# Kernel tuning notes

Hardware: AMD Instinct MI355X
Metric: run time of the kernel (lower is better)

## Reference

```python
import jax, jax.numpy as jnp
import numpy as np

N, E, F, H, G, C = 50000, 800000, 768, 256, 512, 2  # H = nhid*2 (nhid=128), G graphs, C classes
NHID = 128


def setup_inputs() -> dict:
    key = jax.random.key(0)
    ks = jax.random.split(key, 18)
    s = 0.05
    x = jax.random.normal(ks[0], (N, F), jnp.float32)
    edge_index = jax.random.randint(ks[1], (2, E), 0, N, dtype=jnp.int32)
    # sorted batch vector; every graph non-empty so the 'first node per graph' gather is valid
    batch = ((jnp.arange(N) * G) // N).astype(jnp.int32)
    return {
        "x": x,
        "edge_index": edge_index,
        "batch": batch,
        # GATConv 1 (in=F, out=H, heads=1)
        "W1": jax.random.normal(ks[2], (F, H), jnp.float32) * s,
        "as1": jax.random.normal(ks[3], (H,), jnp.float32) * s,
        "ad1": jax.random.normal(ks[4], (H,), jnp.float32) * s,
        "b1": jnp.zeros((H,), jnp.float32),
        # GATConv 2 (in=H, out=H)
        "W2": jax.random.normal(ks[5], (H, H), jnp.float32) * s,
        "as2": jax.random.normal(ks[6], (H,), jnp.float32) * s,
        "ad2": jax.random.normal(ks[7], (H,), jnp.float32) * s,
        "b2": jnp.zeros((H,), jnp.float32),
        # fc0: num_features -> nhid (news branch)
        "W0": jax.random.normal(ks[8], (F, NHID), jnp.float32) * s,
        "b0": jnp.zeros((NHID,), jnp.float32),
        # fc1: 2*nhid -> nhid (used twice, as in the source)
        "Wf1": jax.random.normal(ks[9], (H, NHID), jnp.float32) * s,
        "bf1": jnp.zeros((NHID,), jnp.float32),
        # fc2: nhid -> num_classes
        "Wf2": jax.random.normal(ks[10], (NHID, C), jnp.float32) * s,
        "bf2": jnp.zeros((C,), jnp.float32),
    }


def _gat(x, src, dst, W, a_s, a_d, b):
    # PyG GATConv, heads=1, concat=True, negative_slope=0.2, self-loops pre-appended to src/dst.
    h = x @ W                                   # [N, H]
    e = jax.nn.leaky_relu((h @ a_s)[src] + (h @ a_d)[dst], 0.2)  # [E+N]
    m = jax.ops.segment_max(e, dst, num_segments=N)
    ex = jnp.exp(e - m[dst])                    # stable segment softmax numerator
    denom = jax.ops.segment_sum(ex, dst, num_segments=N)
    agg = jax.ops.segment_sum(ex[:, None] * h[src], dst, num_segments=N)  # [N, H]
    return agg / denom[:, None] + b


def reference(x, edge_index, batch, W1, as1, ad1, b1, W2, as2, ad2, b2, W0, b0, Wf1, bf1, Wf2, bf2):
    loop = jnp.arange(N, dtype=edge_index.dtype)
    src = jnp.concatenate([edge_index[0], loop])  # add self-loops (PyG default)
    dst = jnp.concatenate([edge_index[1], loop])
    h = jax.nn.selu(_gat(x, src, dst, W1, as1, ad1, b1))
    h = jax.nn.selu(_gat(h, src, dst, W2, as2, ad2, b2))
    # global mean pool over graphs
    cnt = jax.ops.segment_sum(jnp.ones((N,), h.dtype), batch, num_segments=G)
    pooled = jax.nn.selu(jax.ops.segment_sum(h, batch, num_segments=G) / cnt[:, None])
    z = jax.nn.selu(pooled @ Wf1 + bf1)
    # dropout(p=0.5) in eval mode -> identity
    # concat branch: first node of each graph (news root)
    first_idx = jax.ops.segment_min(jnp.arange(N), batch, num_segments=G)
    news = jax.nn.relu(x[first_idx] @ W0 + b0)
    z = jnp.concatenate([z, news], axis=1)       # [G, 2*nhid]
    z = jax.nn.relu(z @ Wf1 + bf1)
    return jax.nn.log_softmax(z @ Wf2 + bf2, axis=-1)
```

## Files before the change

kernel.cpp:

```cpp
#include <hip/hip_runtime.h>
#include <hip/hip_bf16.h>
#include <cstdint>
#include <cstddef>

#define NN 50000
#define EE 800000
#define FF 768
#define HH 256
#define GG 512
#define CC 2
#define NHIDD 128
#define ETOT (EE + NN)
#define NCHUNK 49

typedef __attribute__((ext_vector_type(8))) short bf16x8;
typedef __attribute__((ext_vector_type(4))) float f32x4;
typedef __attribute__((ext_vector_type(8))) unsigned short us8;

__device__ __forceinline__ float b2f(unsigned short u){
  union { float f; uint32_t i; } v; v.i = ((uint32_t)u) << 16; return v.f;
}
__device__ __forceinline__ unsigned short f2b(float f){
  uint32_t u = __float_as_uint(f);
  uint32_t r = (u + 0x7fffu + ((u >> 16) & 1u)) >> 16;
  return (unsigned short)r;
}
__device__ __forceinline__ uint32_t cvtpk(float a, float b){
  uint32_t d;
  asm volatile("v_cvt_pk_bf16_f32 %0, %1, %2" : "=v"(d) : "v"(a), "v"(b));
  return d;
}
__device__ __forceinline__ float selu_f(float x){
  const float lam = 1.0507009873554805f, alp = 1.6732632423543772f;
  return x > 0.f ? lam * x : lam * alp * (__expf(x) - 1.f);
}

__device__ __forceinline__ void gload_lds16(const void* g, void* l){
  __builtin_amdgcn_global_load_lds((const __attribute__((address_space(1))) void*)g,
                                   (__attribute__((address_space(3))) void*)l, 16, 0, 0);
}

__global__ __launch_bounds__(256) void swizzleW2(const float* __restrict__ W1, const float* __restrict__ W2,
                                                 unsigned short* __restrict__ Wsw1, unsigned short* __restrict__ Wsw2){
  int i = blockIdx.x * 256 + threadIdx.x;
  if (i < FF * HH){
    int k = i / HH, n = i % HH;
    Wsw1[(size_t)(k >> 5) * 8192 + n * 32 + (k & 31)] = f2b(W1[i]);
  } else {
    int i2 = i - FF * HH;
    int k = i2 / HH, n = i2 % HH;
    Wsw2[(size_t)(k >> 5) * 8192 + n * 32 + (k & 31)] = f2b(W2[i2]);
  }
}

__global__ __launch_bounds__(256) void deg_kernel(const int* __restrict__ dstA, int* __restrict__ deg){
  int i = blockIdx.x * 256 + threadIdx.x;
  if (i < ETOT){
    int d = (i < EE) ? dstA[i] : (i - EE);
    atomicAdd(&deg[d], 1);
  }
}

__global__ __launch_bounds__(256) void scanA(const int* __restrict__ deg, int* __restrict__ bsum){
  __shared__ int red[256];
  int c = blockIdx.x, tid = threadIdx.x;
  int base = c * 1024 + tid * 4;
  int s = 0;
#pragma unroll
  for (int j = 0; j < 4; j++){ int idx = base + j; if (idx < NN) s += deg[idx]; }
  red[tid] = s; __syncthreads();
  for (int off = 128; off > 0; off >>= 1){
    if (tid < off) red[tid] += red[tid + off];
    __syncthreads();
  }
  if (tid == 0) bsum[c] = red[0];
}

__global__ __launch_bounds__(256) void scanC(const int* __restrict__ deg, const int* __restrict__ bsum,
                                             int* __restrict__ row_ptr, int* __restrict__ fill_ptr){
  __shared__ int ts[256];
  __shared__ int cbase;
  int c = blockIdx.x, tid = threadIdx.x;
  int pb = (tid < c) ? bsum[tid] : 0;
  ts[tid] = pb; __syncthreads();
  for (int off = 128; off > 0; off >>= 1){
    if (tid < off) ts[tid] += ts[tid + off];
    __syncthreads();
  }
  if (tid == 0) cbase = ts[0];
  __syncthreads();
  int base = c * 1024 + tid * 4;
  int v[4]; int s = 0;
#pragma unroll
  for (int j = 0; j < 4; j++){ int idx = base + j; v[j] = (idx < NN) ? deg[idx] : 0; s += v[j]; }
  ts[tid] = s; __syncthreads();
  for (int off = 1; off < 256; off <<= 1){
    int add = (tid >= off) ? ts[tid - off] : 0;
    __syncthreads();
    ts[tid] += add;
    __syncthreads();
  }
  int run = ts[tid] - s + cbase;
#pragma unroll
  for (int j = 0; j < 4; j++){
    int idx = base + j;
    if (idx < NN){ row_ptr[idx] = run; fill_ptr[idx] = run; }
    run += v[j];
  }
  if (c == 0 && tid == 0) row_ptr[NN] = ETOT;
}

__global__ __launch_bounds__(256) void fill_kernel(const int* __restrict__ srcA, const int* __restrict__ dstA,
                                                   int* __restrict__ fill_ptr, int* __restrict__ csr_src){
  int i = blockIdx.x * 256 + threadIdx.x;
  if (i < ETOT){
    int s = (i < EE) ? srcA[i] : (i - EE);
    int d = (i < EE) ? dstA[i] : (i - EE);
    int pos = atomicAdd(&fill_ptr[d], 1);
    csr_src[pos] = s;
  }
}

__global__ __launch_bounds__(512, 4) void gemm1_f32(const float* __restrict__ A,
                                                 const unsigned short* __restrict__ Wsw,
                                                 const float* __restrict__ a_s, const float* __restrict__ a_d,
                                                 unsigned short* __restrict__ out,
                                                 float* __restrict__ als, float* __restrict__ ald, int M){
  __shared__ float Alf[32 * 384];
  const int tid = threadIdx.x;
  const int m0 = blockIdx.x * 32;
  const int lane = tid & 63, w = tid >> 6;
  const int koff = (lane >> 4) * 8;
  const int arow = lane & 15;
  const int nrow = w * 32 + (lane & 15);

  f32x4 acc[2][2];
#pragma unroll
  for (int rt = 0; rt < 2; rt++)
#pragma unroll
    for (int ct = 0; ct < 2; ct++) acc[rt][ct] = (f32x4){0.f, 0.f, 0.f, 0.f};

  const unsigned short* bbase = Wsw + ((size_t)nrow * 32 + koff);
  bf16x8 bcur[2][2];

  auto stage_half = [&](int p){
#pragma unroll
    for (int j = 0; j < 6; j++){
      int L16 = j * 512 + tid;
      int row = L16 / 96;
      int ch  = L16 - row * 96;
      int sch = ch ^ (row & 7);
      int gr  = m0 + row; if (gr >= M) gr = M - 1;
      gload_lds16(A + (size_t)gr * FF + p * 384 + sch * 4,
                  Alf + (size_t)(j * 512 + w * 64) * 4);
    }
  };

#pragma unroll
  for (int p = 0; p < 2; p++){
    if (p == 1) __syncthreads();
    stage_half(p);
#pragma unroll
    for (int k2 = 0; k2 < 2; k2++)
#pragma unroll
      for (int ct = 0; ct < 2; ct++)
        bcur[k2][ct] = *(const bf16x8*)(bbase + (size_t)(p * 12 + k2) * 8192 + ct * 512);
    __syncthreads();

    for (int ks = 0; ks < 6; ks++){
      bf16x8 bnext[2][2];
      if (ks + 1 < 6){
#pragma unroll
        for (int k2 = 0; k2 < 2; k2++)
#pragma unroll
          for (int ct = 0; ct < 2; ct++)
            bnext[k2][ct] = *(const bf16x8*)(bbase + (size_t)(p * 12 + (ks + 1) * 2 + k2) * 8192 + ct * 512);
      }
      bf16x8 af[2][2];
#pragma unroll
      for (int k2 = 0; k2 < 2; k2++)
#pragma unroll
        for (int rt = 0; rt < 2; rt++){
          int R = rt * 16 + arow;
          int c = ks * 16 + k2 * 8 + (lane >> 4) * 2;
          int m = R & 7;
          float4 v0 = *(const float4*)&Alf[R * 384 + ((c)     ^ m) * 4];
          float4 v1 = *(const float4*)&Alf[R * 384 + ((c + 1) ^ m) * 4];
          union { bf16x8 v; uint32_t u[4]; } X;
          X.u[0] = cvtpk(v0.x, v0.y); X.u[1] = cvtpk(v0.z, v0.w);
          X.u[2] = cvtpk(v1.x, v1.y); X.u[3] = cvtpk(v1.z, v1.w);
          af[k2][rt] = X.v;
        }
#pragma unroll
      for (int k2 = 0; k2 < 2; k2++)
#pragma unroll
        for (int rt = 0; rt < 2; rt++)
#pragma unroll
          for (int ct = 0; ct < 2; ct++)
            acc[rt][ct] = __builtin_amdgcn_mfma_f32_16x16x32_bf16(af[k2][rt], bcur[k2][ct], acc[rt][ct], 0, 0, 0);
      if (ks + 1 < 6){
#pragma unroll
        for (int k2 = 0; k2 < 2; k2++)
#pragma unroll
          for (int ct = 0; ct < 2; ct++) bcur[k2][ct] = bnext[k2][ct];
      }
    }
  }

#pragma unroll
  for (int rt = 0; rt < 2; rt++){
    int mbase = m0 + rt * 16 + (lane >> 4) * 4;
#pragma unroll
    for (int r = 0; r < 4; r++){
      int m = mbase + r;
      if (m < M){
        size_t ro = (size_t)m * HH + w * 32 + (lane & 15);
        out[ro + 0]  = f2b(acc[rt][0][r]);
        out[ro + 16] = f2b(acc[rt][1][r]);
      }
    }
  }

  float as_c[2], ad_c[2];
#pragma unroll
  for (int ct = 0; ct < 2; ct++){
    int col = w * 32 + ct * 16 + (lane & 15);
    as_c[ct] = a_s[col]; ad_c[ct] = a_d[col];
  }
  float ps[2][4], pd[2][4];
#pragma unroll
  for (int rt = 0; rt < 2; rt++)
#pragma unroll
    for (int r = 0; r < 4; r++){
      float s = 0.f, d = 0.f;
#pragma unroll
      for (int ct = 0; ct < 2; ct++){ float v = acc[rt][ct][r]; s += v * as_c[ct]; d += v * ad_c[ct]; }
      ps[rt][r] = s; pd[rt][r] = d;
    }
#pragma unroll
  for (int off = 1; off < 16; off <<= 1){
#pragma unroll
    for (int rt = 0; rt < 2; rt++)
#pragma unroll
      for (int r = 0; r < 4; r++){
        ps[rt][r] += __shfl_xor(ps[rt][r], off);
        pd[rt][r] += __shfl_xor(pd[rt][r], off);
      }
  }
  __syncthreads();
  float* red = Alf;
  if ((lane & 15) == 0){
    int q = lane >> 4;
#pragma unroll
    for (int rt = 0; rt < 2; rt++)
#pragma unroll
      for (int r = 0; r < 4; r++){
        int row = rt * 16 + q * 4 + r;
        red[w * 32 + row]       = ps[rt][r];
        red[256 + w * 32 + row] = pd[rt][r];
      }
  }
  __syncthreads();
  if (tid < 32){
    float s = 0.f, d = 0.f;
#pragma unroll
    for (int ww = 0; ww < 8; ww++){
      s += red[ww * 32 + tid];
      d += red[256 + ww * 32 + tid];
    }
    int m = m0 + tid;
    if (m < M){ als[m] = s; ald[m] = d; }
  }
}

template<int K, int MINW>
__global__ __launch_bounds__(256, MINW) void gemm_mfma(const unsigned short* __restrict__ A,
                                                 const unsigned short* __restrict__ Wsw,
                                                 const float* __restrict__ a_s, const float* __restrict__ a_d,
                                                 unsigned short* __restrict__ out,
                                                 float* __restrict__ als, float* __restrict__ ald, int M){
  constexpr int CHROW = K / 8;
  __shared__ unsigned short Al[32 * K];
  const int tid = threadIdx.x;
  const int m0 = blockIdx.x * 32;
  const int lane = tid & 63, w = tid >> 6;
  const int koff = (lane >> 4) * 8;
  const int arow = lane & 15;
  const int nrow = w * 64 + (lane & 15);

  f32x4 acc[2][4];
#pragma unroll
  for (int rt = 0; rt < 2; rt++)
#pragma unroll
    for (int ct = 0; ct < 4; ct++) acc[rt][ct] = (f32x4){0.f, 0.f, 0.f, 0.f};

  constexpr int ROUNDS = (32 * CHROW) / 256;
#pragma unroll
  for (int j = 0; j < ROUNDS; j++){
    int L16 = j * 256 + tid;
    int row = L16 / CHROW;
    int ch  = L16 - row * CHROW;
    int sch = ch ^ (row & 7);
    int gr  = m0 + row; if (gr >= M) gr = M - 1;
    gload_lds16(A + (size_t)gr * K + sch * 8,
                &Al[(size_t)(j * 256 + w * 64) * 8]);
  }

  const unsigned short* bbase = Wsw + ((size_t)nrow * 32 + koff);
  bf16x8 bcur[2][4];
#pragma unroll
  for (int k2 = 0; k2 < 2; k2++)
#pragma unroll
    for (int ct = 0; ct < 4; ct++)
      bcur[k2][ct] = *(const bf16x8*)(bbase + (size_t)k2 * 8192 + ct * 512);

  __syncthreads();

  constexpr int NIT = K / 64;
  for (int ks = 0; ks < NIT; ks++){
    bf16x8 bnext[2][4];
    if (ks + 1 < NIT){
#pragma unroll
      for (int k2 = 0; k2 < 2; k2++)
#pragma unroll
        for (int ct = 0; ct < 4; ct++)
          bnext[k2][ct] = *(const bf16x8*)(bbase + (size_t)((ks + 1) * 2 + k2) * 8192 + ct * 512);
    }
    bf16x8 af[2][2];
#pragma unroll
    for (int k2 = 0; k2 < 2; k2++)
#pragma unroll
      for (int rt = 0; rt < 2; rt++){
        int R = rt * 16 + arow;
        int chb = (ks * 8 + k2 * 4 + (lane >> 4)) ^ (R & 7);
        af[k2][rt] = *(const bf16x8*)&Al[(size_t)R * K + chb * 8];
      }
#pragma unroll
    for (int k2 = 0; k2 < 2; k2++)
#pragma unroll
      for (int rt = 0; rt < 2; rt++)
#pragma unroll
        for (int ct = 0; ct < 4; ct++)
          acc[rt][ct] = __builtin_amdgcn_mfma_f32_16x16x32_bf16(af[k2][rt], bcur[k2][ct], acc[rt][ct], 0, 0, 0);
    if (ks + 1 < NIT){
#pragma unroll
      for (int k2 = 0; k2 < 2; k2++)
#pragma unroll
        for (int ct = 0; ct < 4; ct++) bcur[k2][ct] = bnext[k2][ct];
    }
  }

#pragma unroll
  for (int rt = 0; rt < 2; rt++){
    int mbase = m0 + rt * 16 + (lane >> 4) * 4;
#pragma unroll
    for (int r = 0; r < 4; r++){
      int m = mbase + r;
      if (m < M){
        size_t ro = (size_t)m * HH + w * 64 + (lane & 15);
        out[ro + 0]  = f2b(acc[rt][0][r]);
        out[ro + 16] = f2b(acc[rt][1][r]);
        out[ro + 32] = f2b(acc[rt][2][r]);
        out[ro + 48] = f2b(acc[rt][3][r]);
      }
    }
  }

  float as_c[4], ad_c[4];
#pragma unroll
  for (int ct = 0; ct < 4; ct++){
    int col = w * 64 + ct * 16 + (lane & 15);
    as_c[ct] = a_s[col]; ad_c[ct] = a_d[col];
  }
  float ps[2][4], pd[2][4];
#pragma unroll
  for (int rt = 0; rt < 2; rt++)
#pragma unroll
    for (int r = 0; r < 4; r++){
      float s = 0.f, d = 0.f;
#pragma unroll
      for (int ct = 0; ct < 4; ct++){ float v = acc[rt][ct][r]; s += v * as_c[ct]; d += v * ad_c[ct]; }
      ps[rt][r] = s; pd[rt][r] = d;
    }
#pragma unroll
  for (int off = 1; off < 16; off <<= 1){
#pragma unroll
    for (int rt = 0; rt < 2; rt++)
#pragma unroll
      for (int r = 0; r < 4; r++){
        ps[rt][r] += __shfl_xor(ps[rt][r], off);
        pd[rt][r] += __shfl_xor(pd[rt][r], off);
      }
  }
  __syncthreads();
  float* red = (float*)Al;
  if ((lane & 15) == 0){
    int q = lane >> 4;
#pragma unroll
    for (int rt = 0; rt < 2; rt++)
#pragma unroll
      for (int r = 0; r < 4; r++){
        int row = rt * 16 + q * 4 + r;
        red[w * 32 + row]       = ps[rt][r];
        red[128 + w * 32 + row] = pd[rt][r];
      }
  }
  __syncthreads();
  if (tid < 32){
    float s = red[tid] + red[32 + tid] + red[64 + tid] + red[96 + tid];
    float d = red[128 + tid] + red[160 + tid] + red[192 + tid] + red[224 + tid];
    int m = m0 + tid;
    if (m < M){ als[m] = s; ald[m] = d; }
  }
}

__global__ __launch_bounds__(256) void agg_wave(const unsigned short* __restrict__ h,
    const float* __restrict__ als, const float* __restrict__ ald,
    const int* __restrict__ row_ptr, const int* __restrict__ csr_src,
    const float* __restrict__ bias, unsigned short* __restrict__ outp){
  int node = blockIdx.x * 4 + (threadIdx.x >> 6);
  int lane = threadIdx.x & 63;
  if (node >= NN) return;
  int base = row_ptr[node];
  int deg  = row_ptr[node + 1] - base;
  float aldd = ald[node];
  float den = 0.f;
  float a[8] = {0.f, 0.f, 0.f, 0.f, 0.f, 0.f, 0.f, 0.f};
  const int f8 = (lane & 31) * 8;
  const int half = lane >> 5;
  for (int p0 = 0; p0 < deg; p0 += 64){
    int cnt = min(64, deg - p0);
    float ev = 0.f; int s = 0;
    if (lane < cnt){
      s = csr_src[base + p0 + lane];
      float v = als[s] + aldd;
      v = v > 0.f ? v : 0.2f * v;
      ev = __expf(v);
    }
    den += ev;
    int j = 0;
    for (; j + 8 <= cnt; j += 8){
      int j0 = j + half, j1 = j + 2 + half, j2 = j + 4 + half, j3 = j + 6 + half;
      int s0 = __shfl(s, j0), s1 = __shfl(s, j1), s2 = __shfl(s, j2), s3 = __shfl(s, j3);
      float e0 = __shfl(ev, j0), e1 = __shfl(ev, j1), e2 = __shfl(ev, j2), e3 = __shfl(ev, j3);
      us8 g0 = *(const us8*)&h[(size_t)s0 * HH + f8];
      us8 g1 = *(const us8*)&h[(size_t)s1 * HH + f8];
      us8 g2 = *(const us8*)&h[(size_t)s2 * HH + f8];
      us8 g3 = *(const us8*)&h[(size_t)s3 * HH + f8];
#pragma unroll
      for (int i = 0; i < 8; i++) a[i] += e0 * b2f(g0[i]) + e1 * b2f(g1[i]);
#pragma unroll
      for (int i = 0; i < 8; i++) a[i] += e2 * b2f(g2[i]) + e3 * b2f(g3[i]);
    }
    for (; j + 4 <= cnt; j += 4){
      int j0 = j + half, j1 = j + 2 + half;
      int s0 = __shfl(s, j0), s1 = __shfl(s, j1);
      float e0 = __shfl(ev, j0), e1 = __shfl(ev, j1);
      us8 g0 = *(const us8*)&h[(size_t)s0 * HH + f8];
      us8 g1 = *(const us8*)&h[(size_t)s1 * HH + f8];
#pragma unroll
      for (int i = 0; i < 8; i++) a[i] += e0 * b2f(g0[i]) + e1 * b2f(g1[i]);
    }
    for (; j < cnt; j += 2){
      int jj = j + half;
      int sj = __shfl(s, jj & 63);
      float ejr = __shfl(ev, jj & 63);
      float ej = (jj < cnt) ? ejr : 0.f;
      us8 gj = *(const us8*)&h[(size_t)sj * HH + f8];
#pragma unroll
      for (int i = 0; i < 8; i++) a[i] += ej * b2f(gj[i]);
    }
  }
  for (int off = 32; off > 0; off >>= 1) den += __shfl_xor(den, off);
#pragma unroll
  for (int i = 0; i < 8; i++) a[i] += __shfl_xor(a[i], 32);
  if (lane < 32){
    float inv = 1.f / den;
    float4 b4a = *(const float4*)&bias[f8];
    float4 b4b = *(const float4*)&bias[f8 + 4];
    us8 o;
    o[0] = f2b(selu_f(a[0] * inv + b4a.x));
    o[1] = f2b(selu_f(a[1] * inv + b4a.y));
    o[2] = f2b(selu_f(a[2] * inv + b4a.z));
    o[3] = f2b(selu_f(a[3] * inv + b4a.w));
    o[4] = f2b(selu_f(a[4] * inv + b4b.x));
    o[5] = f2b(selu_f(a[5] * inv + b4b.y));
    o[6] = f2b(selu_f(a[6] * inv + b4b.z));
    o[7] = f2b(selu_f(a[7] * inv + b4b.w));
    *(us8*)&outp[(size_t)node * HH + f8] = o;
  }
}

__global__ __launch_bounds__(256) void head_kernel(const unsigned short* __restrict__ x3,
    const int* __restrict__ batch, const float* __restrict__ x,
    const float* __restrict__ W0, const float* __restrict__ b0,
    const float* __restrict__ Wf1, const float* __restrict__ bf1,
    const float* __restrict__ Wf2, const float* __restrict__ bf2,
    float* __restrict__ out){
  __shared__ float pr[HH];
  __shared__ float xr[FF];
  __shared__ float zc[HH];
  __shared__ int se[2];
  __shared__ float l0s[2], l1s[2];
  int g = blockIdx.x, t = threadIdx.x;
  if (t < 2){
    int target = g + t, lo = 0, hi = NN;
    while (lo < hi){ int mid = (lo + hi) >> 1; if (batch[mid] < target) lo = mid + 1; else hi = mid; }
    se[t] = lo;
  }
  __syncthreads();
  int s = se[0], e = se[1];
  {
    float acc = 0.f;
    for (int n = s; n < e; n++) acc += b2f(x3[(size_t)n * HH + t]);
    pr[t] = selu_f(acc / (float)(e - s));
  }
  for (int k = t; k < FF; k += 256) xr[k] = x[(size_t)s * FF + k];
  __syncthreads();
  if (t < NHIDD){
    float acc = 0.f;
    for (int k = 0; k < HH; k++) acc += pr[k] * Wf1[k * NHIDD + t];
    zc[t] = selu_f(acc + bf1[t]);
  } else {
    int t2 = t - NHIDD;
    float acc = 0.f;
    for (int k = 0; k < FF; k++) acc += xr[k] * W0[k * NHIDD + t2];
    acc += b0[t2];
    zc[NHIDD + t2] = acc > 0.f ? acc : 0.f;
  }
  __syncthreads();
  if (t < NHIDD){
    float acc = 0.f;
    for (int k = 0; k < HH; k++) acc += zc[k] * Wf1[k * NHIDD + t];
    float z2 = acc + bf1[t]; z2 = z2 > 0.f ? z2 : 0.f;
    float p0 = z2 * Wf2[t * CC + 0];
    float p1 = z2 * Wf2[t * CC + 1];
    for (int off = 32; off > 0; off >>= 1){ p0 += __shfl_xor(p0, off); p1 += __shfl_xor(p1, off); }
    if ((t & 63) == 0){ l0s[t >> 6] = p0; l1s[t >> 6] = p1; }
  }
  __syncthreads();
  if (t == 0){
    float l0 = l0s[0] + l0s[1] + bf2[0];
    float l1 = l1s[0] + l1s[1] + bf2[1];
    float mx = fmaxf(l0, l1);
    float lse = mx + logf(__expf(l0 - mx) + __expf(l1 - mx));
    out[g * CC + 0] = l0 - lse;
    out[g * CC + 1] = l1 - lse;
  }
}

extern "C" void kernel_launch(void* const* d_in, const int* in_sizes, int n_in,
                              void* d_out, int out_size, void* d_ws, size_t ws_size,
                              hipStream_t stream){
  const float* x          = (const float*)d_in[0];
  const int* edge_index   = (const int*)d_in[1];
  const int* batch        = (const int*)d_in[2];
  const float* W1  = (const float*)d_in[3];
  const float* as1 = (const float*)d_in[4];
  const float* ad1 = (const float*)d_in[5];
  const float* b1  = (const float*)d_in[6];
  const float* W2  = (const float*)d_in[7];
  const float* as2 = (const float*)d_in[8];
  const float* ad2 = (const float*)d_in[9];
  const float* b2  = (const float*)d_in[10];
  const float* W0  = (const float*)d_in[11];
  const float* b0  = (const float*)d_in[12];
  const float* Wf1 = (const float*)d_in[13];
  const float* bf1 = (const float*)d_in[14];
  const float* Wf2 = (const float*)d_in[15];
  const float* bf2 = (const float*)d_in[16];
  float* out = (float*)d_out;

  char* w = (char*)d_ws;
  size_t off = 0;
  auto alloc = [&](size_t bytes){ size_t o = off; off += (bytes + 255) & ~(size_t)255; return o; };
  unsigned short* h    = (unsigned short*)(w + alloc((size_t)NN * HH * 2));
  unsigned short* x2   = (unsigned short*)(w + alloc((size_t)NN * HH * 2));
  unsigned short* Wsw1 = (unsigned short*)(w + alloc((size_t)FF * HH * 2));
  unsigned short* Wsw2 = (unsigned short*)(w + alloc((size_t)HH * HH * 2));
  float* als     = (float*)(w + alloc((size_t)NN * 4));
  float* ald     = (float*)(w + alloc((size_t)NN * 4));
  int*   deg     = (int*)(w + alloc((size_t)NN * 4));
  int*   row_ptr = (int*)(w + alloc((size_t)(NN + 1) * 4));
  int*   fillp   = (int*)(w + alloc((size_t)NN * 4));
  int*   csr_src = (int*)(w + alloc((size_t)ETOT * 4));
  int*   bsum    = (int*)(w + alloc(64 * 4));

  const int* srcA = edge_index;
  const int* dstA = edge_index + EE;

  swizzleW2<<<(FF * HH + HH * HH) / 256, 256, 0, stream>>>(W1, W2, Wsw1, Wsw2);

  hipMemsetAsync(deg, 0, (size_t)NN * 4, stream);
  deg_kernel<<<(ETOT + 255) / 256, 256, 0, stream>>>(dstA, deg);
  scanA<<<NCHUNK, 256, 0, stream>>>(deg, bsum);
  scanC<<<NCHUNK, 256, 0, stream>>>(deg, bsum, row_ptr, fillp);
  fill_kernel<<<(ETOT + 255) / 256, 256, 0, stream>>>(srcA, dstA, fillp, csr_src);

  const int gemm_grid = (NN + 31) / 32;
  gemm1_f32<<<gemm_grid, 512, 0, stream>>>(x, Wsw1, as1, ad1, h, als, ald, NN);
  agg_wave<<<(NN + 3) / 4, 256, 0, stream>>>(h, als, ald, row_ptr, csr_src, b1, x2);
  gemm_mfma<HH, 3><<<gemm_grid, 256, 0, stream>>>(x2, Wsw2, as2, ad2, h, als, ald, NN);
  agg_wave<<<(NN + 3) / 4, 256, 0, stream>>>(h, als, ald, row_ptr, csr_src, b2, x2);
  head_kernel<<<GG, 256, 0, stream>>>(x2, batch, x, W0, b0, Wf1, bf1, Wf2, bf2, out);
}
```

Baseline: 576.6 us.

## Merge scan passes, reorder B loads before A staging, vectorize head pooling

Removes the separate scanA kernel launch: each scanC block recomputes its prefix base by summing all preceding degree entries directly, which trades one launch for redundant reads (up to about 49K ints per block). In gemm1 the B-fragment register loads are issued before the async A staging instead of after. The head kernel's mean-pool now splits nodes across 8 warp-groups with 16-byte bf16 vector loads and reduces partial sums through shared memory, replacing a per-thread scalar serial loop.

```diff
diff --git a/kernel.cpp b/kernel.cpp
--- a/kernel.cpp
+++ b/kernel.cpp
@@ -61,28 +61,15 @@
   }
 }
 
-__global__ __launch_bounds__(256) void scanA(const int* __restrict__ deg, int* __restrict__ bsum){
-  __shared__ int red[256];
-  int c = blockIdx.x, tid = threadIdx.x;
-  int base = c * 1024 + tid * 4;
-  int s = 0;
-#pragma unroll
-  for (int j = 0; j < 4; j++){ int idx = base + j; if (idx < NN) s += deg[idx]; }
-  red[tid] = s; __syncthreads();
-  for (int off = 128; off > 0; off >>= 1){
-    if (tid < off) red[tid] += red[tid + off];
-    __syncthreads();
-  }
-  if (tid == 0) bsum[c] = red[0];
-}
-
-__global__ __launch_bounds__(256) void scanC(const int* __restrict__ deg, const int* __restrict__ bsum,
+__global__ __launch_bounds__(256) void scanC(const int* __restrict__ deg,
                                              int* __restrict__ row_ptr, int* __restrict__ fill_ptr){
   __shared__ int ts[256];
   __shared__ int cbase;
   int c = blockIdx.x, tid = threadIdx.x;
-  int pb = (tid < c) ? bsum[tid] : 0;
-  ts[tid] = pb; __syncthreads();
+  int psum = 0;
+  int lim = c * 1024;
+  for (int i = tid; i < lim; i += 256) psum += deg[i];
+  ts[tid] = psum; __syncthreads();
   for (int off = 128; off > 0; off >>= 1){
     if (tid < off) ts[tid] += ts[tid + off];
     __syncthreads();
@@ -159,12 +146,12 @@
 #pragma unroll
   for (int p = 0; p < 2; p++){
     if (p == 1) __syncthreads();
-    stage_half(p);
 #pragma unroll
     for (int k2 = 0; k2 < 2; k2++)
 #pragma unroll
       for (int ct = 0; ct < 2; ct++)
         bcur[k2][ct] = *(const bf16x8*)(bbase + (size_t)(p * 12 + k2) * 8192 + ct * 512);
+    stage_half(p);
     __syncthreads();
 
     for (int ks = 0; ks < 6; ks++){
@@ -497,6 +484,7 @@
     const float* __restrict__ Wf1, const float* __restrict__ bf1,
     const float* __restrict__ Wf2, const float* __restrict__ bf2,
     float* __restrict__ out){
+  __shared__ float prp[8][HH];
   __shared__ float pr[HH];
   __shared__ float xr[FF];
   __shared__ float zc[HH];
@@ -511,11 +499,25 @@
   __syncthreads();
   int s = se[0], e = se[1];
   {
+    int f8g = (t & 31) * 8;
+    int ns  = t >> 5;
+    float pa[8] = {0.f,0.f,0.f,0.f,0.f,0.f,0.f,0.f};
+    for (int n = s + ns; n < e; n += 8){
+      us8 v = *(const us8*)&x3[(size_t)n * HH + f8g];
+#pragma unroll
+      for (int i = 0; i < 8; i++) pa[i] += b2f(v[i]);
+    }
+#pragma unroll
+    for (int i = 0; i < 8; i++) prp[ns][f8g + i] = pa[i];
+  }
+  for (int k = t; k < FF; k += 256) xr[k] = x[(size_t)s * FF + k];
+  __syncthreads();
+  {
     float acc = 0.f;
-    for (int n = s; n < e; n++) acc += b2f(x3[(size_t)n * HH + t]);
+#pragma unroll
+    for (int ww = 0; ww < 8; ww++) acc += prp[ww][t];
     pr[t] = selu_f(acc / (float)(e - s));
   }
-  for (int k = t; k < FF; k += 256) xr[k] = x[(size_t)s * FF + k];
   __syncthreads();
   if (t < NHIDD){
     float acc = 0.f;
@@ -584,7 +586,6 @@
   int*   row_ptr = (int*)(w + alloc((size_t)(NN + 1) * 4));
   int*   fillp   = (int*)(w + alloc((size_t)NN * 4));
   int*   csr_src = (int*)(w + alloc((size_t)ETOT * 4));
-  int*   bsum    = (int*)(w + alloc(64 * 4));
 
   const int* srcA = edge_index;
   const int* dstA = edge_index + EE;
@@ -593,8 +594,7 @@
 
   hipMemsetAsync(deg, 0, (size_t)NN * 4, stream);
   deg_kernel<<<(ETOT + 255) / 256, 256, 0, stream>>>(dstA, deg);
-  scanA<<<NCHUNK, 256, 0, stream>>>(deg, bsum);
-  scanC<<<NCHUNK, 256, 0, stream>>>(deg, bsum, row_ptr, fillp);
+  scanC<<<NCHUNK, 256, 0, stream>>>(deg, row_ptr, fillp);
   fill_kernel<<<(ETOT + 255) / 256, 256, 0, stream>>>(srcA, dstA, fillp, csr_src);
 
   const int gemm_grid = (NN + 31) / 32;
```

Measured after the change: 582.3 us. Within noise of the previous version (+1.0%).
